# Kernel tuning notes

Measured on AMD Instinct MI355X. Metric: run time of the kernel, lower is better.

## Reference

```python
import jax, jax.numpy as jnp
import numpy as np

D_MODEL = 1024
N_HEADS = 16
D_K = D_MODEL // N_HEADS
SCALE = float(np.sqrt(D_K))


def setup_inputs() -> dict:
    key = jax.random.key(0)
    ks = jax.random.split(key, 11)
    B, L, D = 2, 2048, D_MODEL
    s = 1.0 / np.sqrt(D)
    inp = {
        "q": jax.random.normal(ks[0], (B, L, D), dtype=jnp.float32),
        "k": jax.random.normal(ks[1], (B, L, D), dtype=jnp.float32),
        "v": jax.random.normal(ks[2], (B, L, D), dtype=jnp.float32),
        "Wq": jax.random.normal(ks[3], (D, D), dtype=jnp.float32) * s,
        "bq": jnp.zeros((D,), dtype=jnp.float32),
        "Wk": jax.random.normal(ks[4], (D, D), dtype=jnp.float32) * s,
        "bk": jnp.zeros((D,), dtype=jnp.float32),
        "Wv": jax.random.normal(ks[5], (D, D), dtype=jnp.float32) * s,
        "bv": jnp.zeros((D,), dtype=jnp.float32),
        "Wo": jax.random.normal(ks[6], (D, D), dtype=jnp.float32) * s,
        "bo": jnp.zeros((D,), dtype=jnp.float32),
    }
    return inp


def reference(q, k, v, Wq, bq, Wk, bk, Wv, bv, Wo, bo):
    B, L, D = q.shape
    H, Dk = N_HEADS, D_K
    # projections: [B,L,D] -> [B,H,L,Dk]
    def proj(x, W, b):
        y = x @ W + b
        return y.reshape(B, -1, H, Dk).transpose(0, 2, 1, 3)
    qh = proj(q, Wq, bq)
    kh = proj(k, Wk, bk)
    vh = proj(v, Wv, bv)
    # scores [B,H,Lq,Lk]
    scores = jnp.einsum("bhqd,bhkd->bhqk", qh, kh) / SCALE
    attn = jax.nn.softmax(scores, axis=-1)  # dropout=0.0 -> identity
    out = jnp.einsum("bhqk,bhkd->bhqd", attn, vh)
    out = out.transpose(0, 2, 1, 3).reshape(B, -1, D)
    return out @ Wo + bo
```

## Files before the change

kernel.cpp:

```cpp
#include <hip/hip_runtime.h>
#include <hip/hip_bf16.h>
#include <stdint.h>
#include <stddef.h>

typedef unsigned short ushortT;
typedef __attribute__((ext_vector_type(8))) short bf16x8s;
typedef __attribute__((ext_vector_type(4))) float f32x4;


__device__ __forceinline__ short f2bf(float f) {
  unsigned u = __float_as_uint(f);
  u += 0x7FFFu + ((u >> 16) & 1u);
  return (short)(u >> 16);
}

__device__ __forceinline__ unsigned pk_bf16(float a, float b) {
  __hip_bfloat162 h = __float22bfloat162_rn(make_float2(a, b));
  return *(unsigned*)&h;
}

__device__ __forceinline__ bf16x8s cvt8(const float* src) {
  const float4* p = (const float4*)src;
  float4 a = p[0], b = p[1];
  bf16x8s r;
  r[0] = f2bf(a.x); r[1] = f2bf(a.y); r[2] = f2bf(a.z); r[3] = f2bf(a.w);
  r[4] = f2bf(b.x); r[5] = f2bf(b.y); r[6] = f2bf(b.z); r[7] = f2bf(b.w);
  return r;
}

__device__ __forceinline__ void load_lds16(const ushortT* g, ushortT* l) {
  __builtin_amdgcn_global_load_lds(
      (const __attribute__((address_space(1))) void*)(g),
      (__attribute__((address_space(3))) void*)(l), 16, 0, 0);
}

__global__ __launch_bounds__(256)
void prep(const float* __restrict__ q, const float* __restrict__ k,
          const float* __restrict__ v,
          const float* __restrict__ Wq, const float* __restrict__ Wk,
          const float* __restrict__ Wv, const float* __restrict__ Wo,
          ushortT* __restrict__ Qc, ushortT* __restrict__ Kc,
          ushortT* __restrict__ Vc, ushortT* __restrict__ Wt)
{
  const int z = blockIdx.z;
  if (z < 4) {
    if (blockIdx.x >= 1024) return;
    __shared__ __align__(16) ushortT t[32][33];
    const float* W = (z == 0) ? Wq : (z == 1) ? Wk : (z == 2) ? Wv : Wo;
    ushortT* dst = Wt + (size_t)z * 1024 * 1024;
    const int x = (blockIdx.x & 31) * 32, y = (blockIdx.x >> 5) * 32;
    const int tx = threadIdx.x & 31, ty = threadIdx.x >> 5;
#pragma unroll
    for (int i = ty; i < 32; i += 8)
      t[i][tx] = (ushortT)f2bf(W[(size_t)(y + i) * 1024 + x + tx]);
    __syncthreads();
#pragma unroll
    for (int i = ty; i < 32; i += 8)
      dst[(size_t)(x + i) * 1024 + y + tx] = t[tx][i];
  } else {
    const float* src = (z == 4) ? q : (z == 5) ? k : v;
    ushortT* dst = (z == 4) ? Qc : (z == 5) ? Kc : Vc;
    const size_t i8 = ((size_t)blockIdx.x * 256 + threadIdx.x) * 8;
    *(bf16x8s*)(dst + i8) = cvt8(src + i8);
  }
}

__device__ __forceinline__ void gemm_core_128(
    const ushortT* __restrict__ A, const ushortT* __restrict__ Bt,
    int K, ushortT* As, ushortT* Bs, f32x4 (&acc)[4][4], int m0, int n0)
{
  const int tid  = threadIdx.x;
  const int wave = tid >> 6, lane = tid & 63;
  const int wm = (wave & 1) << 6;
  const int wn = (wave >> 1) << 6;
  const int lr = lane & 15;
  const int lk = (lane >> 4) << 3;

#pragma unroll
  for (int mi = 0; mi < 4; ++mi)
#pragma unroll
    for (int ni = 0; ni < 4; ++ni)
      acc[mi][ni] = (f32x4){0.f, 0.f, 0.f, 0.f};

  for (int k0 = 0; k0 < K; k0 += 32) {
    __syncthreads();
#pragma unroll
    for (int i = 0; i < 2; ++i) {
      const int cc  = tid + (i << 8);
      const int row = cc >> 2;
      const int ko  = (cc & 3) << 3;
      load_lds16(A  + (size_t)(m0 + row) * K + k0 + ko, As + cc * 8);
      load_lds16(Bt + (size_t)(n0 + row) * K + k0 + ko, Bs + cc * 8);
    }
    __syncthreads();

    bf16x8s af[4], bfr[4];
#pragma unroll
    for (int i = 0; i < 4; ++i)
      af[i] = *(const bf16x8s*)(As + (wm + i * 16 + lr) * 32 + lk);
#pragma unroll
    for (int i = 0; i < 4; ++i)
      bfr[i] = *(const bf16x8s*)(Bs + (wn + i * 16 + lr) * 32 + lk);

#pragma unroll
    for (int mi = 0; mi < 4; ++mi)
#pragma unroll
      for (int ni = 0; ni < 4; ++ni)
        acc[mi][ni] = __builtin_amdgcn_mfma_f32_16x16x32_bf16(
            af[mi], bfr[ni], acc[mi][ni], 0, 0, 0);
  }
}

__global__ __launch_bounds__(256)
void proj_gemm(const ushortT* __restrict__ Qc, const ushortT* __restrict__ Kc,
               const ushortT* __restrict__ Vc, const ushortT* __restrict__ WtAll,
               const float* __restrict__ bq, const float* __restrict__ bk,
               const float* __restrict__ bv,
               ushortT* __restrict__ Qh, ushortT* __restrict__ Kh,
               ushortT* __restrict__ Vt)
{
  __shared__ __align__(16) ushortT As[128 * 32];
  __shared__ __align__(16) ushortT Bs[128 * 32];
  const int which = blockIdx.z;
  const ushortT* A  = (which == 0) ? Qc : (which == 1) ? Kc : Vc;
  const ushortT* Bt = WtAll + (size_t)which * 1024 * 1024;
  const float* bias = (which == 0) ? bq : (which == 1) ? bk : bv;
  const int m0 = blockIdx.x * 128, n0 = blockIdx.y * 128;

  f32x4 acc[4][4];
  gemm_core_128(A, Bt, 1024, As, Bs, acc, m0, n0);

  const int lane = threadIdx.x & 63, wave = threadIdx.x >> 6;
  const int wm = (wave & 1) << 6, wn = (wave >> 1) << 6;
  const int lr = lane & 15, quad = lane >> 4;
  const float QSCALE = 0.18033688011112042f;

#pragma unroll
  for (int ni = 0; ni < 4; ++ni) {
    const int n = n0 + wn + ni * 16 + lr;
    const float bias_v = bias[n];
    const int h = n >> 6, d = n & 63;
#pragma unroll
    for (int mi = 0; mi < 4; ++mi) {
#pragma unroll
      for (int r = 0; r < 4; ++r) {
        const int m = m0 + wm + mi * 16 + quad * 4 + r;
        const int b = m >> 11, l = m & 2047;
        float val = acc[mi][ni][r] + bias_v;
        if (which == 0) val *= QSCALE;
        const ushortT o = (ushortT)f2bf(val);
        const size_t bh = (size_t)(b * 16 + h);
        if (which == 0)      Qh[(bh * 2048 + l) * 64 + d] = o;
        else if (which == 1) Kh[(bh * 2048 + l) * 64 + d] = o;
        else                 Vt[(bh * 64 + d) * 2048 + l] = o;
      }
    }
  }
}

__global__ __launch_bounds__(256)
void attn_kernel(const ushortT* __restrict__ Qh, const ushortT* __restrict__ Kh,
                 const ushortT* __restrict__ Vt, ushortT* __restrict__ Ob)
{
  const int b = blockIdx.z, h = blockIdx.y, qt = blockIdx.x;
  const int bh = b * 16 + h;
  const int wave = threadIdx.x >> 6, lane = threadIdx.x & 63;
  const int lr = lane & 15, quad = lane >> 4, lk = quad * 8;
  const int q0 = qt * 64 + wave * 16;

  const ushortT* Q = Qh + ((size_t)bh * 2048 + q0) * 64;
  const ushortT* K = Kh + (size_t)bh * 2048 * 64;
  const ushortT* V = Vt + (size_t)bh * 64 * 2048;

  __shared__ __align__(16) ushortT Ks[64 * 76];
  __shared__ __align__(16) ushortT Vs[64 * 76];
  __shared__ __align__(16) ushortT P4[4][16 * 88];
  ushortT* Pw = P4[wave];

  const bf16x8s qf0 = *(const bf16x8s*)(Q + lr * 64 + lk);
  const bf16x8s qf1 = *(const bf16x8s*)(Q + lr * 64 + 32 + lk);

  f32x4 o[4];
#pragma unroll
  for (int nt = 0; nt < 4; ++nt) o[nt] = (f32x4){0.f, 0.f, 0.f, 0.f};
  float lsum = 0.f;

  const int tid = threadIdx.x;
  const int srow = tid >> 3;
  const int sc8  = (tid & 7) << 3;

  for (int kt = 0; kt < 2048; kt += 64) {
    bf16x8s kch[2], vch[2];
#pragma unroll
    for (int i = 0; i < 2; ++i) {
      const int row = srow + i * 32;
      kch[i] = *(const bf16x8s*)(K + (size_t)(kt + row) * 64 + sc8);
      vch[i] = *(const bf16x8s*)(V + (size_t)row * 2048 + kt + sc8);
    }
    __syncthreads();
#pragma unroll
    for (int i = 0; i < 2; ++i) {
      const int row = srow + i * 32;
      *(bf16x8s*)(Ks + row * 76 + sc8) = kch[i];
      *(bf16x8s*)(Vs + row * 76 + sc8) = vch[i];
    }
    __syncthreads();

    f32x4 s[4];
#pragma unroll
    for (int t = 0; t < 4; ++t) s[t] = (f32x4){0.f, 0.f, 0.f, 0.f};
#pragma unroll
    for (int t = 0; t < 4; ++t) {
      const bf16x8s kf0 = *(const bf16x8s*)(Ks + (t * 16 + lr) * 76 + lk);
      const bf16x8s kf1 = *(const bf16x8s*)(Ks + (t * 16 + lr) * 76 + 32 + lk);
      s[t] = __builtin_amdgcn_mfma_f32_16x16x32_bf16(kf0, qf0, s[t], 0, 0, 0);
      s[t] = __builtin_amdgcn_mfma_f32_16x16x32_bf16(kf1, qf1, s[t], 0, 0, 0);
    }

#pragma unroll
    for (int t = 0; t < 4; ++t) {
      const float e0 = __builtin_amdgcn_exp2f(s[t][0]);
      const float e1 = __builtin_amdgcn_exp2f(s[t][1]);
      const float e2 = __builtin_amdgcn_exp2f(s[t][2]);
      const float e3 = __builtin_amdgcn_exp2f(s[t][3]);
      lsum += (e0 + e1) + (e2 + e3);
      uint2 d;
      d.x = pk_bf16(e0, e1);
      d.y = pk_bf16(e2, e3);
      *(uint2*)(Pw + lr * 88 + t * 16 + quad * 4) = d;
    }
    asm volatile("s_waitcnt lgkmcnt(0)" ::: "memory");

    const bf16x8s pf0 = *(const bf16x8s*)(Pw + lr * 88 + lk);
    const bf16x8s pf1 = *(const bf16x8s*)(Pw + lr * 88 + 32 + lk);
#pragma unroll
    for (int nt = 0; nt < 4; ++nt) {
      const bf16x8s vf0 = *(const bf16x8s*)(Vs + (nt * 16 + lr) * 76 + lk);
      const bf16x8s vf1 = *(const bf16x8s*)(Vs + (nt * 16 + lr) * 76 + 32 + lk);
      o[nt] = __builtin_amdgcn_mfma_f32_16x16x32_bf16(pf0, vf0, o[nt], 0, 0, 0);
      o[nt] = __builtin_amdgcn_mfma_f32_16x16x32_bf16(pf1, vf1, o[nt], 0, 0, 0);
    }
  }

  float* fP = (float*)Pw;
  {
    float s = lsum;
    s += __shfl_xor(s, 16);
    s += __shfl_xor(s, 32);
    fP[lr] = 1.0f / s;
  }
  asm volatile("s_waitcnt lgkmcnt(0)" ::: "memory");
  float invr[4];
#pragma unroll
  for (int r = 0; r < 4; ++r) invr[r] = fP[quad * 4 + r];

#pragma unroll
  for (int nt = 0; nt < 4; ++nt) {
    const int dcol = h * 64 + nt * 16 + lr;
#pragma unroll
    for (int r = 0; r < 4; ++r) {
      const int l = q0 + quad * 4 + r;
      Ob[((size_t)b * 2048 + l) * 1024 + dcol] = (ushortT)f2bf(o[nt][r] * invr[r]);
    }
  }
}

__global__ __launch_bounds__(256)
void out_gemm(const ushortT* __restrict__ Ob, const ushortT* __restrict__ Wto,
              const float* __restrict__ bo, float* __restrict__ C)
{
  __shared__ __align__(16) ushortT As[128 * 32];
  __shared__ __align__(16) ushortT Bs[128 * 32];
  const int m0 = blockIdx.x * 128, n0 = blockIdx.y * 128;

  f32x4 acc[4][4];
  gemm_core_128(Ob, Wto, 1024, As, Bs, acc, m0, n0);

  const int lane = threadIdx.x & 63, wave = threadIdx.x >> 6;
  const int wm = (wave & 1) << 6, wn = (wave >> 1) << 6;
  const int lr = lane & 15, quad = lane >> 4;

#pragma unroll
  for (int ni = 0; ni < 4; ++ni) {
    const int n = n0 + wn + ni * 16 + lr;
    const float bias_v = bo[n];
#pragma unroll
    for (int mi = 0; mi < 4; ++mi) {
#pragma unroll
      for (int r = 0; r < 4; ++r) {
        const int m = m0 + wm + mi * 16 + quad * 4 + r;
        C[(size_t)m * 1024 + n] = acc[mi][ni][r] + bias_v;
      }
    }
  }
}

extern "C" void kernel_launch(void* const* d_in, const int* in_sizes, int n_in,
                              void* d_out, int out_size, void* d_ws, size_t ws_size,
                              hipStream_t stream) {
  const float* q  = (const float*)d_in[0];
  const float* k  = (const float*)d_in[1];
  const float* v  = (const float*)d_in[2];
  const float* Wq = (const float*)d_in[3];
  const float* bq = (const float*)d_in[4];
  const float* Wk = (const float*)d_in[5];
  const float* bk = (const float*)d_in[6];
  const float* Wv = (const float*)d_in[7];
  const float* bv = (const float*)d_in[8];
  const float* Wo = (const float*)d_in[9];
  const float* bo = (const float*)d_in[10];

  char* ws = (char*)d_ws;
  ushortT* Wt = (ushortT*)(ws);
  ushortT* Qh = (ushortT*)(ws + (size_t)(8  << 20));
  ushortT* Kh = (ushortT*)(ws + (size_t)(16 << 20));
  ushortT* Vt = (ushortT*)(ws + (size_t)(24 << 20));
  ushortT* Qc = (ushortT*)(ws + (size_t)(32 << 20));
  ushortT* Kc = (ushortT*)(ws + (size_t)(40 << 20));
  ushortT* Vc = (ushortT*)(ws + (size_t)(48 << 20));
  ushortT* Ob = Qc;

  prep<<<dim3(2048, 1, 7), 256, 0, stream>>>(q, k, v, Wq, Wk, Wv, Wo,
                                             Qc, Kc, Vc, Wt);
  proj_gemm<<<dim3(32, 8, 3), 256, 0, stream>>>(Qc, Kc, Vc, Wt, bq, bk, bv,
                                                Qh, Kh, Vt);
  attn_kernel<<<dim3(32, 16, 2), 256, 0, stream>>>(Qh, Kh, Vt, Ob);
  out_gemm<<<dim3(32, 8), 256, 0, stream>>>(Ob, Wt + (size_t)3 * 1024 * 1024,
                                            bo, (float*)d_out);
}
```

Before: 243.2 us.

## Fuse fp32-to-bf16 input conversion into projection GEMM and retile output GEMM

```diff
diff --git a/kernel.cpp b/kernel.cpp
--- a/kernel.cpp
+++ b/kernel.cpp
@@ -35,39 +35,28 @@
 }
 
 __global__ __launch_bounds__(256)
-void prep(const float* __restrict__ q, const float* __restrict__ k,
-          const float* __restrict__ v,
-          const float* __restrict__ Wq, const float* __restrict__ Wk,
+void prep(const float* __restrict__ Wq, const float* __restrict__ Wk,
           const float* __restrict__ Wv, const float* __restrict__ Wo,
-          ushortT* __restrict__ Qc, ushortT* __restrict__ Kc,
-          ushortT* __restrict__ Vc, ushortT* __restrict__ Wt)
-{
+          ushortT* __restrict__ Wt)
+{
+  __shared__ __align__(16) ushortT t[32][33];
   const int z = blockIdx.z;
-  if (z < 4) {
-    if (blockIdx.x >= 1024) return;
-    __shared__ __align__(16) ushortT t[32][33];
-    const float* W = (z == 0) ? Wq : (z == 1) ? Wk : (z == 2) ? Wv : Wo;
-    ushortT* dst = Wt + (size_t)z * 1024 * 1024;
-    const int x = (blockIdx.x & 31) * 32, y = (blockIdx.x >> 5) * 32;
-    const int tx = threadIdx.x & 31, ty = threadIdx.x >> 5;
-#pragma unroll
-    for (int i = ty; i < 32; i += 8)
-      t[i][tx] = (ushortT)f2bf(W[(size_t)(y + i) * 1024 + x + tx]);
-    __syncthreads();
-#pragma unroll
-    for (int i = ty; i < 32; i += 8)
-      dst[(size_t)(x + i) * 1024 + y + tx] = t[tx][i];
-  } else {
-    const float* src = (z == 4) ? q : (z == 5) ? k : v;
-    ushortT* dst = (z == 4) ? Qc : (z == 5) ? Kc : Vc;
-    const size_t i8 = ((size_t)blockIdx.x * 256 + threadIdx.x) * 8;
-    *(bf16x8s*)(dst + i8) = cvt8(src + i8);
-  }
-}
-
-__device__ __forceinline__ void gemm_core_128(
-    const ushortT* __restrict__ A, const ushortT* __restrict__ Bt,
-    int K, ushortT* As, ushortT* Bs, f32x4 (&acc)[4][4], int m0, int n0)
+  const float* W = (z == 0) ? Wq : (z == 1) ? Wk : (z == 2) ? Wv : Wo;
+  ushortT* dst = Wt + (size_t)z * 1024 * 1024;
+  const int x = (blockIdx.x & 31) * 32, y = (blockIdx.x >> 5) * 32;
+  const int tx = threadIdx.x & 31, ty = threadIdx.x >> 5;
+#pragma unroll
+  for (int i = ty; i < 32; i += 8)
+    t[i][tx] = (ushortT)f2bf(W[(size_t)(y + i) * 1024 + x + tx]);
+  __syncthreads();
+#pragma unroll
+  for (int i = ty; i < 32; i += 8)
+    dst[(size_t)(x + i) * 1024 + y + tx] = t[tx][i];
+}
+
+__device__ __forceinline__ void gemm_core_f32A(
+    const float* __restrict__ A, const ushortT* __restrict__ Bt,
+    ushortT* As, ushortT* Bs, f32x4 (&acc)[4][4], int m0, int n0)
 {
   const int tid  = threadIdx.x;
   const int wave = tid >> 6, lane = tid & 63;
@@ -82,15 +71,23 @@
     for (int ni = 0; ni < 4; ++ni)
       acc[mi][ni] = (f32x4){0.f, 0.f, 0.f, 0.f};
 
-  for (int k0 = 0; k0 < K; k0 += 32) {
-    __syncthreads();
+  for (int k0 = 0; k0 < 1024; k0 += 32) {
+    bf16x8s av[2];
 #pragma unroll
     for (int i = 0; i < 2; ++i) {
       const int cc  = tid + (i << 8);
       const int row = cc >> 2;
       const int ko  = (cc & 3) << 3;
-      load_lds16(A  + (size_t)(m0 + row) * K + k0 + ko, As + cc * 8);
-      load_lds16(Bt + (size_t)(n0 + row) * K + k0 + ko, Bs + cc * 8);
+      av[i] = cvt8(A + (size_t)(m0 + row) * 1024 + k0 + ko);
+    }
+    __syncthreads();
+#pragma unroll
+    for (int i = 0; i < 2; ++i) {
+      const int cc = tid + (i << 8);
+      *(bf16x8s*)(As + cc * 8) = av[i];
+      const int row = cc >> 2;
+      const int ko  = (cc & 3) << 3;
+      load_lds16(Bt + (size_t)(n0 + row) * 1024 + k0 + ko, Bs + cc * 8);
     }
     __syncthreads();
 
@@ -112,8 +109,8 @@
 }
 
 __global__ __launch_bounds__(256)
-void proj_gemm(const ushortT* __restrict__ Qc, const ushortT* __restrict__ Kc,
-               const ushortT* __restrict__ Vc, const ushortT* __restrict__ WtAll,
+void proj_gemm(const float* __restrict__ q, const float* __restrict__ k,
+               const float* __restrict__ v, const ushortT* __restrict__ WtAll,
                const float* __restrict__ bq, const float* __restrict__ bk,
                const float* __restrict__ bv,
                ushortT* __restrict__ Qh, ushortT* __restrict__ Kh,
@@ -122,13 +119,13 @@
   __shared__ __align__(16) ushortT As[128 * 32];
   __shared__ __align__(16) ushortT Bs[128 * 32];
   const int which = blockIdx.z;
-  const ushortT* A  = (which == 0) ? Qc : (which == 1) ? Kc : Vc;
+  const float* A    = (which == 0) ? q  : (which == 1) ? k  : v;
   const ushortT* Bt = WtAll + (size_t)which * 1024 * 1024;
   const float* bias = (which == 0) ? bq : (which == 1) ? bk : bv;
   const int m0 = blockIdx.x * 128, n0 = blockIdx.y * 128;
 
   f32x4 acc[4][4];
-  gemm_core_128(A, Bt, 1024, As, Bs, acc, m0, n0);
+  gemm_core_f32A(A, Bt, As, Bs, acc, m0, n0);
 
   const int lane = threadIdx.x & 63, wave = threadIdx.x >> 6;
   const int wm = (wave & 1) << 6, wn = (wave >> 1) << 6;
@@ -270,18 +267,58 @@
               const float* __restrict__ bo, float* __restrict__ C)
 {
   __shared__ __align__(16) ushortT As[128 * 32];
-  __shared__ __align__(16) ushortT Bs[128 * 32];
-  const int m0 = blockIdx.x * 128, n0 = blockIdx.y * 128;
-
-  f32x4 acc[4][4];
-  gemm_core_128(Ob, Wto, 1024, As, Bs, acc, m0, n0);
-
-  const int lane = threadIdx.x & 63, wave = threadIdx.x >> 6;
-  const int wm = (wave & 1) << 6, wn = (wave >> 1) << 6;
-  const int lr = lane & 15, quad = lane >> 4;
-
-#pragma unroll
-  for (int ni = 0; ni < 4; ++ni) {
+  __shared__ __align__(16) ushortT Bs[64 * 32];
+  const int m0 = blockIdx.x * 128, n0 = blockIdx.y * 64;
+
+  const int tid  = threadIdx.x;
+  const int wave = tid >> 6, lane = tid & 63;
+  const int wm = (wave & 1) << 6;
+  const int wn = (wave >> 1) << 5;
+  const int lr = lane & 15;
+  const int lk = (lane >> 4) << 3;
+
+  f32x4 acc[4][2];
+#pragma unroll
+  for (int mi = 0; mi < 4; ++mi)
+#pragma unroll
+    for (int ni = 0; ni < 2; ++ni)
+      acc[mi][ni] = (f32x4){0.f, 0.f, 0.f, 0.f};
+
+  for (int k0 = 0; k0 < 1024; k0 += 32) {
+    __syncthreads();
+#pragma unroll
+    for (int i = 0; i < 2; ++i) {
+      const int cc  = tid + (i << 8);
+      const int row = cc >> 2;
+      const int ko  = (cc & 3) << 3;
+      load_lds16(Ob + (size_t)(m0 + row) * 1024 + k0 + ko, As + cc * 8);
+    }
+    {
+      const int row = tid >> 2;
+      const int ko  = (tid & 3) << 3;
+      load_lds16(Wto + (size_t)(n0 + row) * 1024 + k0 + ko, Bs + tid * 8);
+    }
+    __syncthreads();
+
+    bf16x8s af[4], bfr[2];
+#pragma unroll
+    for (int i = 0; i < 4; ++i)
+      af[i] = *(const bf16x8s*)(As + (wm + i * 16 + lr) * 32 + lk);
+#pragma unroll
+    for (int i = 0; i < 2; ++i)
+      bfr[i] = *(const bf16x8s*)(Bs + (wn + i * 16 + lr) * 32 + lk);
+
+#pragma unroll
+    for (int mi = 0; mi < 4; ++mi)
+#pragma unroll
+      for (int ni = 0; ni < 2; ++ni)
+        acc[mi][ni] = __builtin_amdgcn_mfma_f32_16x16x32_bf16(
+            af[mi], bfr[ni], acc[mi][ni], 0, 0, 0);
+  }
+
+  const int quad = lane >> 4;
+#pragma unroll
+  for (int ni = 0; ni < 2; ++ni) {
     const int n = n0 + wn + ni * 16 + lr;
     const float bias_v = bo[n];
 #pragma unroll
@@ -315,16 +352,12 @@
   ushortT* Qh = (ushortT*)(ws + (size_t)(8  << 20));
   ushortT* Kh = (ushortT*)(ws + (size_t)(16 << 20));
   ushortT* Vt = (ushortT*)(ws + (size_t)(24 << 20));
-  ushortT* Qc = (ushortT*)(ws + (size_t)(32 << 20));
-  ushortT* Kc = (ushortT*)(ws + (size_t)(40 << 20));
-  ushortT* Vc = (ushortT*)(ws + (size_t)(48 << 20));
-  ushortT* Ob = Qc;
-
-  prep<<<dim3(2048, 1, 7), 256, 0, stream>>>(q, k, v, Wq, Wk, Wv, Wo,
-                                             Qc, Kc, Vc, Wt);
-  proj_gemm<<<dim3(32, 8, 3), 256, 0, stream>>>(Qc, Kc, Vc, Wt, bq, bk, bv,
+  ushortT* Ob = (ushortT*)(ws + (size_t)(32 << 20));
+
+  prep<<<dim3(1024, 1, 4), 256, 0, stream>>>(Wq, Wk, Wv, Wo, Wt);
+  proj_gemm<<<dim3(32, 8, 3), 256, 0, stream>>>(q, k, v, Wt, bq, bk, bv,
                                                 Qh, Kh, Vt);
   attn_kernel<<<dim3(32, 16, 2), 256, 0, stream>>>(Qh, Kh, Vt, Ob);
-  out_gemm<<<dim3(32, 8), 256, 0, stream>>>(Ob, Wt + (size_t)3 * 1024 * 1024,
-                                            bo, (float*)d_out);
-}
+  out_gemm<<<dim3(32, 16), 256, 0, stream>>>(Ob, Wt + (size_t)3 * 1024 * 1024,
+                                             bo, (float*)d_out);
+}
```

Result: slower. 255.6 us (+5.1%).
